# Optimization experiments

Measured on AMD Instinct MI355X. Metric: run time of the kernel, lower is better.

The kernel has to match this reference:

```python
import jax, jax.numpy as jnp
import numpy as np

B, I, D = 4, 8192, 1024
R_MIN, R_MAX = 0.4, 0.99


def setup_inputs() -> dict:
    key = jax.random.key(0)
    k_x, k_u = jax.random.split(key)
    x = jax.random.normal(k_x, (B, I, D), dtype=jnp.float32)
    # nu_logs initialized as in LRU.__init__: ring-uniform radii in [r_min, r_max]
    u = jax.random.uniform(k_u, (D,), dtype=jnp.float32)
    nus = -jnp.log(u * (R_MAX**2 - R_MIN**2) + R_MIN**2) / 2.0
    nu_logs = jnp.log(nus)
    return {"x": x, "nu_logs": nu_logs}


def reference(x, nu_logs):
    # lambdas in (0,1): per-channel decay; gammas normalize input magnitude
    lambdas = jnp.exp(-jnp.exp(nu_logs))            # [d]
    gammas = jnp.sqrt(1.0 - jnp.abs(lambdas) ** 2)  # [d]
    values = gammas[None, None, :] * x              # [b, i, d]
    a = jnp.broadcast_to(lambdas[None, None, :], values.shape)  # [b, i, d]

    # inclusive discounted cumsum (left-to-right): h_t = lambda * h_{t-1} + v_t
    def combine(c1, c2):
        a1, b1 = c1
        a2, b2 = c2
        return (a1 * a2, a2 * b1 + b2)

    _, hidden = jax.lax.associative_scan(combine, (a, values), axis=1)
    return hidden  # [b, i, d]
```

## Files before the change

### kernel.cpp

```cpp
#include <hip/hip_runtime.h>
#include <math.h>


#define B_  4
#define I_  8192
#define D_  1024
#define C_  256
#define L_  32
#define D4  (D_ / 4)

typedef float f32x4 __attribute__((ext_vector_type(4)));

__device__ __forceinline__ void load_lam_gam(const float* __restrict__ nu_logs,
                                             int d4, float4& lam, float4& gam) {
    const float* nl = nu_logs + d4 * 4;
    lam.x = expf(-expf(nl[0]));
    lam.y = expf(-expf(nl[1]));
    lam.z = expf(-expf(nl[2]));
    lam.w = expf(-expf(nl[3]));
    gam.x = sqrtf(1.0f - lam.x * lam.x);
    gam.y = sqrtf(1.0f - lam.y * lam.y);
    gam.z = sqrtf(1.0f - lam.z * lam.z);
    gam.w = sqrtf(1.0f - lam.w * lam.w);
}

__device__ __forceinline__ void step(float4& h, const float4 lam,
                                     const float4 gam, const float4 v) {
    h.x = fmaf(lam.x, h.x, gam.x * v.x);
    h.y = fmaf(lam.y, h.y, gam.y * v.y);
    h.z = fmaf(lam.z, h.z, gam.z * v.z);
    h.w = fmaf(lam.w, h.w, gam.w * v.w);
}

__global__ __launch_bounds__(256) void lru_carry(const float4* __restrict__ x,
                                                 const float* __restrict__ nu_logs,
                                                 float4* __restrict__ carry) {
    int tid = blockIdx.x * 256 + threadIdx.x;
    int d4 = tid & (D4 - 1);
    int c  = (tid >> 8) & (C_ - 1);
    int b  = tid >> 16;

    float4 lam, gam;
    load_lam_gam(nu_logs, d4, lam, gam);

    int idx = (b * I_ + c * L_) * D4 + d4;
    float4 h = {0.f, 0.f, 0.f, 0.f};
#pragma unroll
    for (int tt = 0; tt < L_; tt += 8) {
        float4 v0 = x[idx + 0 * D4];
        float4 v1 = x[idx + 1 * D4];
        float4 v2 = x[idx + 2 * D4];
        float4 v3 = x[idx + 3 * D4];
        float4 v4 = x[idx + 4 * D4];
        float4 v5 = x[idx + 5 * D4];
        float4 v6 = x[idx + 6 * D4];
        float4 v7 = x[idx + 7 * D4];
        step(h, lam, gam, v0);
        step(h, lam, gam, v1);
        step(h, lam, gam, v2);
        step(h, lam, gam, v3);
        step(h, lam, gam, v4);
        step(h, lam, gam, v5);
        step(h, lam, gam, v6);
        step(h, lam, gam, v7);
        idx += 8 * D4;
    }
    carry[(b * C_ + c) * D4 + d4] = h;
}

__global__ __launch_bounds__(256) void lru_scan_out(const float4* __restrict__ x,
                                                    const float* __restrict__ nu_logs,
                                                    const float4* __restrict__ carry,
                                                    float4* __restrict__ out) {
    int tid = blockIdx.x * 256 + threadIdx.x;
    int d4 = tid & (D4 - 1);
    int c  = (tid >> 8) & (C_ - 1);
    int b  = tid >> 16;

    float4 lam, gam;
    load_lam_gam(nu_logs, d4, lam, gam);

    const float* nl = nu_logs + d4 * 4;
    float4 pL;
    pL.x = expf(-expf(nl[0]) * (float)L_);
    pL.y = expf(-expf(nl[1]) * (float)L_);
    pL.z = expf(-expf(nl[2]) * (float)L_);
    pL.w = expf(-expf(nl[3]) * (float)L_);

    int idx = (b * I_ + c * L_) * D4 + d4;

    float4 v[8];
#pragma unroll
    for (int k = 0; k < 8; ++k) v[k] = x[idx + k * D4];

    float4 h = {0.f, 0.f, 0.f, 0.f};
    const float4* cb = carry + b * C_ * D4 + d4;
#pragma unroll 4
    for (int j = 0; j < c; ++j) {
        float4 cj = cb[j * D4];
        h.x = fmaf(pL.x, h.x, cj.x);
        h.y = fmaf(pL.y, h.y, cj.y);
        h.z = fmaf(pL.z, h.z, cj.z);
        h.w = fmaf(pL.w, h.w, cj.w);
    }

#pragma unroll
    for (int tt = 0; tt < L_; tt += 8) {
        float4 w[8];
        if (tt + 8 < L_) {
#pragma unroll
            for (int k = 0; k < 8; ++k) w[k] = x[idx + (8 + k) * D4];
        }
#pragma unroll
        for (int k = 0; k < 8; ++k) {
            step(h, lam, gam, v[k]);
            __builtin_nontemporal_store(*(const f32x4*)&h, (f32x4*)&out[idx + k * D4]);
        }
        if (tt + 8 < L_) {
#pragma unroll
            for (int k = 0; k < 8; ++k) v[k] = w[k];
        }
        idx += 8 * D4;
    }
}

extern "C" void kernel_launch(void* const* d_in, const int* in_sizes, int n_in,
                              void* d_out, int out_size, void* d_ws, size_t ws_size,
                              hipStream_t stream) {
    (void)in_sizes; (void)n_in; (void)out_size; (void)ws_size;
    const float4* x       = (const float4*)d_in[0];
    const float*  nu_logs = (const float*)d_in[1];
    float4*       out     = (float4*)d_out;
    float4*       carry   = (float4*)d_ws;

    dim3 blk(256);
    dim3 grd((B_ * C_ * D4) / 256);

    lru_carry<<<grd, blk, 0, stream>>>(x, nu_logs, carry);
    lru_scan_out<<<grd, blk, 0, stream>>>(x, nu_logs, carry, out);
}
```

Measured before the change: 265.6 us.

## Replace two-pass carry scan with single-pass decoupled look-back scan

The two-kernel scheme (carry pass, then rescan) is replaced with one kernel using decoupled look-back. Blocks take virtual IDs from an atomic counter, publish their chunk aggregate and inclusive prefix with flags, and spin on predecessors to build the prefix. Each block keeps its 32 rows in registers so x is read from global memory only once. This removes a full second read of x and the O(c) serial carry loop, at the cost of inter-block spin-waiting, a small init kernel, and heavy register pressure from 32 float4 values per thread.

```diff
diff --git a/kernel.cpp b/kernel.cpp
--- a/kernel.cpp
+++ b/kernel.cpp
@@ -2,14 +2,21 @@
 #include <math.h>
 
 
-#define B_  4
-#define I_  8192
-#define D_  1024
-#define C_  256
-#define L_  32
-#define D4  (D_ / 4)
+#define B_   4
+#define I_   8192
+#define D_   1024
+#define C_   256
+#define L_   32
+#define D4   (D_ / 4)
+#define NBLK (B_ * C_)
+
+#define FLAG_OFF_U 64
+#define FLAG_STRIDE 16
+#define AGG_OFF_F (32 * 1024)
+#define INC_OFF_F (AGG_OFF_F + NBLK * D_)
 
 typedef float f32x4 __attribute__((ext_vector_type(4)));
+typedef unsigned int uint_t;
 
 __device__ __forceinline__ void load_lam_gam(const float* __restrict__ nu_logs,
                                              int d4, float4& lam, float4& gam) {
@@ -32,54 +39,46 @@
     h.w = fmaf(lam.w, h.w, gam.w * v.w);
 }
 
-__global__ __launch_bounds__(256) void lru_carry(const float4* __restrict__ x,
-                                                 const float* __restrict__ nu_logs,
-                                                 float4* __restrict__ carry) {
-    int tid = blockIdx.x * 256 + threadIdx.x;
-    int d4 = tid & (D4 - 1);
-    int c  = (tid >> 8) & (C_ - 1);
-    int b  = tid >> 16;
+__device__ __forceinline__ float4 pay_load4(const float* p) {
+    float4 r;
+    r.x = __hip_atomic_load(p + 0, __ATOMIC_RELAXED, __HIP_MEMORY_SCOPE_AGENT);
+    r.y = __hip_atomic_load(p + 1, __ATOMIC_RELAXED, __HIP_MEMORY_SCOPE_AGENT);
+    r.z = __hip_atomic_load(p + 2, __ATOMIC_RELAXED, __HIP_MEMORY_SCOPE_AGENT);
+    r.w = __hip_atomic_load(p + 3, __ATOMIC_RELAXED, __HIP_MEMORY_SCOPE_AGENT);
+    return r;
+}
+
+__device__ __forceinline__ void pay_store4(float* p, const float4 v) {
+    __hip_atomic_store(p + 0, v.x, __ATOMIC_RELAXED, __HIP_MEMORY_SCOPE_AGENT);
+    __hip_atomic_store(p + 1, v.y, __ATOMIC_RELAXED, __HIP_MEMORY_SCOPE_AGENT);
+    __hip_atomic_store(p + 2, v.z, __ATOMIC_RELAXED, __HIP_MEMORY_SCOPE_AGENT);
+    __hip_atomic_store(p + 3, v.w, __ATOMIC_RELAXED, __HIP_MEMORY_SCOPE_AGENT);
+}
+
+__global__ __launch_bounds__(256) void lru_init(uint_t* __restrict__ u) {
+    int t = blockIdx.x * 256 + threadIdx.x;
+    if (t == 0) u[0] = 0;
+    if (t < NBLK) u[FLAG_OFF_U + t * FLAG_STRIDE] = 0;
+}
+
+__global__ __launch_bounds__(256) void lru_onepass(const float4* __restrict__ x,
+                                                   const float* __restrict__ nu_logs,
+                                                   uint_t* __restrict__ wu,
+                                                   float* __restrict__ wf,
+                                                   float4* __restrict__ out) {
+    __shared__ uint_t s_vid;
+    __shared__ uint_t s_flag;
+    const int tid = threadIdx.x;
+
+    if (tid == 0) s_vid = atomicAdd(&wu[0], 1u);
+    __syncthreads();
+    const int vid = (int)s_vid;
+    const int c = vid & (C_ - 1);
+    const int b = vid >> 8;
+    const int d4 = tid;
 
     float4 lam, gam;
     load_lam_gam(nu_logs, d4, lam, gam);
-
-    int idx = (b * I_ + c * L_) * D4 + d4;
-    float4 h = {0.f, 0.f, 0.f, 0.f};
-#pragma unroll
-    for (int tt = 0; tt < L_; tt += 8) {
-        float4 v0 = x[idx + 0 * D4];
-        float4 v1 = x[idx + 1 * D4];
-        float4 v2 = x[idx + 2 * D4];
-        float4 v3 = x[idx + 3 * D4];
-        float4 v4 = x[idx + 4 * D4];
-        float4 v5 = x[idx + 5 * D4];
-        float4 v6 = x[idx + 6 * D4];
-        float4 v7 = x[idx + 7 * D4];
-        step(h, lam, gam, v0);
-        step(h, lam, gam, v1);
-        step(h, lam, gam, v2);
-        step(h, lam, gam, v3);
-        step(h, lam, gam, v4);
-        step(h, lam, gam, v5);
-        step(h, lam, gam, v6);
-        step(h, lam, gam, v7);
-        idx += 8 * D4;
-    }
-    carry[(b * C_ + c) * D4 + d4] = h;
-}
-
-__global__ __launch_bounds__(256) void lru_scan_out(const float4* __restrict__ x,
-                                                    const float* __restrict__ nu_logs,
-                                                    const float4* __restrict__ carry,
-                                                    float4* __restrict__ out) {
-    int tid = blockIdx.x * 256 + threadIdx.x;
-    int d4 = tid & (D4 - 1);
-    int c  = (tid >> 8) & (C_ - 1);
-    int b  = tid >> 16;
-
-    float4 lam, gam;
-    load_lam_gam(nu_logs, d4, lam, gam);
-
     const float* nl = nu_logs + d4 * 4;
     float4 pL;
     pL.x = expf(-expf(nl[0]) * (float)L_);
@@ -87,40 +86,75 @@
     pL.z = expf(-expf(nl[2]) * (float)L_);
     pL.w = expf(-expf(nl[3]) * (float)L_);
 
-    int idx = (b * I_ + c * L_) * D4 + d4;
+    const int idx = (b * I_ + c * L_) * D4 + d4;
+    float4 v[L_];
+#pragma unroll
+    for (int t = 0; t < L_; ++t) v[t] = x[idx + t * D4];
 
-    float4 v[8];
+    float4 agg = {0.f, 0.f, 0.f, 0.f};
 #pragma unroll
-    for (int k = 0; k < 8; ++k) v[k] = x[idx + k * D4];
+    for (int t = 0; t < L_; ++t) step(agg, lam, gam, v[t]);
 
-    float4 h = {0.f, 0.f, 0.f, 0.f};
-    const float4* cb = carry + b * C_ * D4 + d4;
-#pragma unroll 4
-    for (int j = 0; j < c; ++j) {
-        float4 cj = cb[j * D4];
-        h.x = fmaf(pL.x, h.x, cj.x);
-        h.y = fmaf(pL.y, h.y, cj.y);
-        h.z = fmaf(pL.z, h.z, cj.z);
-        h.w = fmaf(pL.w, h.w, cj.w);
+    float*  aggp = wf + AGG_OFF_F + vid * D_ + d4 * 4;
+    float*  incp = wf + INC_OFF_F + vid * D_ + d4 * 4;
+    uint_t* flg  = wu + FLAG_OFF_U + vid * FLAG_STRIDE;
+
+    float4 s = {0.f, 0.f, 0.f, 0.f};
+
+    if (c == 0) {
+        pay_store4(incp, agg);
+        __syncthreads();
+        if (tid == 0)
+            __hip_atomic_store(flg, 2u, __ATOMIC_RELEASE, __HIP_MEMORY_SCOPE_AGENT);
+    } else {
+        pay_store4(aggp, agg);
+        __syncthreads();
+        if (tid == 0)
+            __hip_atomic_store(flg, 1u, __ATOMIC_RELEASE, __HIP_MEMORY_SCOPE_AGENT);
+
+        float4 w = {1.f, 1.f, 1.f, 1.f};
+        int j = c - 1;
+        for (;;) {
+            if (tid == 0) {
+                uint_t* fj = wu + FLAG_OFF_U + (vid - (c - j)) * FLAG_STRIDE;
+                uint_t f;
+                do {
+                    f = __hip_atomic_load(fj, __ATOMIC_ACQUIRE, __HIP_MEMORY_SCOPE_AGENT);
+                    if (f == 0u) __builtin_amdgcn_s_sleep(1);
+                } while (f == 0u);
+                s_flag = f;
+            }
+            __syncthreads();
+            const uint_t f = s_flag;
+            __syncthreads();
+            const float* pay = wf + (f == 2u ? INC_OFF_F : AGG_OFF_F)
+                             + (vid - (c - j)) * D_ + d4 * 4;
+            const float4 p = pay_load4(pay);
+            s.x = fmaf(w.x, p.x, s.x);
+            s.y = fmaf(w.y, p.y, s.y);
+            s.z = fmaf(w.z, p.z, s.z);
+            s.w = fmaf(w.w, p.w, s.w);
+            if (f == 2u) break;
+            w.x *= pL.x; w.y *= pL.y; w.z *= pL.z; w.w *= pL.w;
+            if (--j < 0) break;
+        }
+
+        float4 P;
+        P.x = fmaf(pL.x, s.x, agg.x);
+        P.y = fmaf(pL.y, s.y, agg.y);
+        P.z = fmaf(pL.z, s.z, agg.z);
+        P.w = fmaf(pL.w, s.w, agg.w);
+        pay_store4(incp, P);
+        __syncthreads();
+        if (tid == 0)
+            __hip_atomic_store(flg, 2u, __ATOMIC_RELEASE, __HIP_MEMORY_SCOPE_AGENT);
     }
 
+    float4 h = s;
 #pragma unroll
-    for (int tt = 0; tt < L_; tt += 8) {
-        float4 w[8];
-        if (tt + 8 < L_) {
-#pragma unroll
-            for (int k = 0; k < 8; ++k) w[k] = x[idx + (8 + k) * D4];
-        }
-#pragma unroll
-        for (int k = 0; k < 8; ++k) {
-            step(h, lam, gam, v[k]);
-            __builtin_nontemporal_store(*(const f32x4*)&h, (f32x4*)&out[idx + k * D4]);
-        }
-        if (tt + 8 < L_) {
-#pragma unroll
-            for (int k = 0; k < 8; ++k) v[k] = w[k];
-        }
-        idx += 8 * D4;
+    for (int t = 0; t < L_; ++t) {
+        step(h, lam, gam, v[t]);
+        __builtin_nontemporal_store(*(const f32x4*)&h, (f32x4*)&out[idx + t * D4]);
     }
 }
 
@@ -131,11 +165,9 @@
     const float4* x       = (const float4*)d_in[0];
     const float*  nu_logs = (const float*)d_in[1];
     float4*       out     = (float4*)d_out;
-    float4*       carry   = (float4*)d_ws;
+    uint_t*       wu      = (uint_t*)d_ws;
+    float*        wf      = (float*)d_ws;
 
-    dim3 blk(256);
-    dim3 grd((B_ * C_ * D4) / 256);
-
-    lru_carry<<<grd, blk, 0, stream>>>(x, nu_logs, carry);
-    lru_scan_out<<<grd, blk, 0, stream>>>(x, nu_logs, carry, out);
+    lru_init<<<dim3(NBLK / 256), dim3(256), 0, stream>>>(wu);
+    lru_onepass<<<dim3(NBLK), dim3(256), 0, stream>>>(x, nu_logs, wu, wf, out);
 }
```

Result: slower. 495.5 us (+86.5%).
